# Kernel tuning notes

Measured on AMD Instinct MI355X. Metric: run time of the kernel, lower is better.

The kernel has to match this reference:

```python
import jax, jax.numpy as jnp
import numpy as np

N, E, HS, HBS, L, SH, RBF, T, NZ, NH = 1024, 16384, 128, 32, 5, 25, 32, 50, 10, 4
HD = HS // NH
OUT = 14  # 3x0e + 2x1e + 1x2e -> 3 + 6 + 5
_rng = np.random.default_rng(7)
# fixed Clebsch-Gordan-style coupling tensor and expansion coefficients (deterministic constants)
CG = jnp.asarray((0.1 * _rng.normal(size=(SH, SH, SH))).astype(np.float32))
EXP = jnp.asarray((0.1 * _rng.normal(size=(SH, OUT, OUT))).astype(np.float32))
_SL = [(l * l, 2 * l + 1) for l in range(5)]  # per-l (offset, size) blocks in the 25-dim rep


def _real_sh(d):
    # real spherical harmonics l=0..4 of unit vectors d [E,3] -> [E,25]
    x, y, z = d[:, 0], d[:, 1], d[:, 2]
    x2, y2, z2 = x * x, y * y, z * z
    sh = [0.282095 * jnp.ones_like(x),
          0.488603 * y, 0.488603 * z, 0.488603 * x,
          1.092548 * x * y, 1.092548 * y * z, 0.315392 * (3 * z2 - 1), 1.092548 * x * z, 0.546274 * (x2 - y2),
          0.590044 * y * (3 * x2 - y2), 2.890611 * x * y * z, 0.457046 * y * (5 * z2 - 1),
          0.373176 * z * (5 * z2 - 3), 0.457046 * x * (5 * z2 - 1), 1.445306 * z * (x2 - y2),
          0.590044 * x * (x2 - 3 * y2),
          2.503343 * x * y * (x2 - y2), 1.770131 * y * z * (3 * x2 - y2), 0.946175 * x * y * (7 * z2 - 1),
          0.669047 * y * z * (7 * z2 - 3), 0.105786 * (35 * z2 * z2 - 30 * z2 + 3),
          0.669047 * x * z * (7 * z2 - 3), 0.473087 * (x2 - y2) * (7 * z2 - 1),
          1.770131 * x * z * (x2 - 3 * y2), 0.625836 * (x2 * x2 - 6 * x2 * y2 + y2 * y2)]
    return jnp.stack(sh, axis=-1)


def _rbf(r, cutoff=12.0, alpha=0.5):
    # exponential Bernstein radial basis with cosine cutoff, [E] -> [E,RBF]
    logf = np.concatenate([[0.0], np.cumsum(np.log(np.arange(1, RBF)))])
    logbinom = jnp.asarray((logf[RBF - 1] - logf - logf[::-1]).astype(np.float32))
    k = jnp.arange(RBF, dtype=jnp.float32)
    xr = jnp.exp(-alpha * r)[:, None]
    log1mx = jnp.log1p(-xr + 1e-7)
    b = jnp.exp(logbinom[None] + k[None] * (-alpha * r[:, None]) + (RBF - 1 - k)[None] * log1mx)
    fcut = 0.5 * (jnp.cos(jnp.pi * jnp.clip(r / cutoff, 0.0, 1.0)) + 1.0)
    return b * fcut[:, None]


def _mix(feat, W):
    # per-degree channel mixing: feat [*,C,25], W [5,C,D] -> [*,D,25]
    return jnp.concatenate([jnp.einsum('ncm,cd->ndm', feat[..., o:o + s], W[l])
                            for l, (o, s) in enumerate(_SL)], axis=-1)


def _forward(z, pos, edge_index, batch, t, step, embed, temb_T, temb_H, sig_W1, sig_b1, sig_W2, sig_b2,
             rad_W1, rad_b1, rad_W2, rad_b2, rad_W3, rad_b3, mix_W, Wq, Wk, Wii, Wij, path_ii, path_ij):
    n = z.shape[0]
    e = edge_index.shape[1]
    src, dst = edge_index[0], edge_index[1]
    vec = pos[src] - pos[dst]
    r = jnp.sqrt((vec * vec).sum(-1) + 1e-12)
    dvec = vec / r[:, None]
    rbf = _rbf(r)           # [E,32]
    sh = _real_sh(dvec)     # [E,25]
    nsc = embed[z]          # [N,HS]
    cat = jnp.concatenate([nsc, jnp.tile(temb_T[t][None], (n, 1)), jnp.tile(temb_H[step][None], (n, 1))], axis=-1)
    nsc = jax.nn.relu(cat @ sig_W1 + sig_b1) @ sig_W2 + sig_b2  # sigma_embedding
    x = jnp.zeros((n, HS, SH), jnp.float32).at[:, :, 0].set(nsc)  # scalar-initialized irrep features
    for l in range(L):
        # radial MLP -> per-edge per-channel tensor-product path weights
        h = jax.nn.silu(rbf @ rad_W1[l] + rad_b1[l])
        h = jax.nn.silu(h @ rad_W2[l] + rad_b2[l])
        w = h @ rad_W3[l] + rad_b3[l]                    # [E,HS]
        Tk = jnp.einsum('ej,ijk->eik', sh, CG)           # [E,25,25] CG-coupled SH operator
        msg = jnp.einsum('eci,eik->eck', x[src], Tk) * w[:, :, None]  # per-edge TP message [E,HS,25]
        agg = jax.ops.segment_sum(msg, dst, num_segments=n)
        y = _mix(agg, mix_W[l])
        # equivariant edge attention (scalars drive logits, full irreps are values)
        q = (x[:, :, 0] @ Wq[l]).reshape(n, NH, HD)
        kk = (x[:, :, 0] @ Wk[l]).reshape(n, NH, HD)
        logits = (q[dst] * kk[src]).sum(-1) * (1.0 / float(np.sqrt(HD)))  # [E,NH]
        m = jax.ops.segment_max(logits, dst, num_segments=n)
        m = jnp.where(jnp.isfinite(m), m, 0.0)
        a = jnp.exp(logits - m[dst])
        den = jax.ops.segment_sum(a, dst, num_segments=n)
        alpha = a / (den[dst] + 1e-9)
        v = x[src].reshape(e, NH, HD, SH)
        att = jax.ops.segment_sum(alpha[:, :, None, None] * v, dst, num_segments=n).reshape(n, HS, SH)
        x = x + y + att
        # gate nonlinearity: ssp/silu on scalars, sigmoid gate on higher-l blocks
        g = jax.nn.sigmoid(x[:, :, 0:1])
        x = jnp.concatenate([jax.nn.silu(x[:, :, 0:1]), x[:, :, 1:] * g], axis=-1)
    # expansion to hamiltonian blocks (3x0e+2x1e+1x2e -> 14x14)
    fii = _mix(x, Wii)                    # [N,HBS,25]
    fij = _mix(x[src] + x[dst], Wij)      # [E,HBS,25]
    w_ii = nsc @ path_ii                  # [N,HBS] path weights
    w_ij = jnp.concatenate([nsc[src], nsc[dst]], axis=-1) @ path_ij  # [E,HBS]
    H_ii = jnp.einsum('nd,ndm,mpq->npq', w_ii, fii, EXP)  # [N,14,14]
    H_ij = jnp.einsum('ed,edm,mpq->epq', w_ij, fij, EXP)  # [E,14,14]
    return H_ii, H_ij


def setup_inputs() -> dict:
    key = jax.random.key(0)
    ks = jax.random.split(key, 40)
    def nrm(i, shape, s):
        return (jax.random.normal(ks[i], shape) * s).astype(jnp.float32)
    inp = {}
    inp['z'] = jax.random.randint(ks[0], (N,), 0, NZ)
    inp['pos'] = nrm(1, (N, 3), 3.0)
    inp['edge_index'] = jax.random.randint(ks[2], (2, E), 0, N)
    inp['batch'] = jnp.sort(jax.random.randint(ks[3], (N,), 0, 8))
    inp['t'] = 25
    inp['step'] = 10
    inp['embed'] = nrm(4, (NZ, HS), 1.0)
    inp['temb_T'] = nrm(5, (T, HS), 1.0)
    inp['temb_H'] = nrm(6, (T, HS), 1.0)
    inp['sig_W1'] = nrm(7, (3 * HS, HS), (3 * HS) ** -0.5)
    inp['sig_b1'] = jnp.zeros((HS,), jnp.float32)
    inp['sig_W2'] = nrm(8, (HS, HS), HS ** -0.5)
    inp['sig_b2'] = jnp.zeros((HS,), jnp.float32)
    inp['rad_W1'] = nrm(9, (L, RBF, 64), RBF ** -0.5)
    inp['rad_b1'] = jnp.zeros((L, 64), jnp.float32)
    inp['rad_W2'] = nrm(10, (L, 64, 64), 64 ** -0.5)
    inp['rad_b2'] = jnp.zeros((L, 64), jnp.float32)
    inp['rad_W3'] = nrm(11, (L, 64, HS), 64 ** -0.5)
    inp['rad_b3'] = jnp.zeros((L, HS), jnp.float32)
    inp['mix_W'] = nrm(12, (L, 5, HS, HS), HS ** -0.5)
    inp['Wq'] = nrm(13, (L, HS, HS), HS ** -0.5)
    inp['Wk'] = nrm(14, (L, HS, HS), HS ** -0.5)
    inp['Wii'] = nrm(15, (5, HS, HBS), HS ** -0.5)
    inp['Wij'] = nrm(16, (5, HS, HBS), HS ** -0.5)
    inp['path_ii'] = nrm(17, (HS, HBS), HS ** -0.5)
    inp['path_ij'] = nrm(18, (2 * HS, HBS), (2 * HS) ** -0.5)
    return inp


def reference(z, pos, edge_index, batch, t, step, embed, temb_T, temb_H, sig_W1, sig_b1, sig_W2, sig_b2,
              rad_W1, rad_b1, rad_W2, rad_b2, rad_W3, rad_b3, mix_W, Wq, Wk, Wii, Wij, path_ii, path_ij):
    return _forward(z, pos, edge_index, batch, t, step, embed, temb_T, temb_H, sig_W1, sig_b1, sig_W2, sig_b2,
                    rad_W1, rad_b1, rad_W2, rad_b2, rad_W3, rad_b3, mix_W, Wq, Wk, Wii, Wij, path_ii, path_ij)
```

## Files before the change

kernel.cpp:

```cpp
#include <hip/hip_runtime.h>
#include <cstdint>
#include <cmath>
#include <cstddef>

constexpr int NN   = 1024;
constexpr int NE   = 16384;
constexpr int HSZ  = 128;
constexpr int NSH  = 25;
constexpr int NRBF = 32;
constexpr int NLAY = 5;
constexpr int XSZ  = HSZ * NSH;
constexpr int HII_SZ = NN * 196;


constexpr size_t OFF_CONSTS = 0;
constexpr size_t OFF_X    = 20560;
constexpr size_t OFF_AGG  = OFF_X    + (size_t)NN * XSZ;
constexpr size_t OFF_ATT  = OFF_AGG  + (size_t)NN * XSZ;
constexpr size_t OFF_X0   = OFF_ATT  + (size_t)NN * XSZ;
constexpr size_t OFF_NSC  = OFF_X0   + (size_t)NN * HSZ;
constexpr size_t OFF_Q    = OFF_NSC  + (size_t)NN * HSZ;
constexpr size_t OFF_K    = OFF_Q    + (size_t)NN * HSZ;
constexpr size_t OFF_RBF  = OFF_K    + (size_t)NN * HSZ;
constexpr size_t OFF_SH   = OFF_RBF  + (size_t)NE * NRBF;
constexpr size_t OFF_TK   = OFF_SH   + (size_t)NE * NSH;
constexpr size_t OFF_WRAD = OFF_TK   + (size_t)NE * NSH * NSH;
constexpr size_t OFF_INT  = OFF_WRAD + (size_t)NE * HSZ;
constexpr size_t NEED_BYTES = OFF_INT * 4 + (size_t)(1024 + 1025 + 1024 + 16384) * 4;

namespace qhc {

struct Pcg64 {
  unsigned __int128 state, inc;
  static unsigned __int128 mult() {
    return (((unsigned __int128)2549297995355413924ULL) << 64) | 4865540595714422341ULL;
  }
  void step() { state = state * mult() + inc; }
  uint64_t next64() {
    step();
    uint64_t hi = (uint64_t)(state >> 64), lo = (uint64_t)state;
    uint64_t x = hi ^ lo;
    unsigned rot = (unsigned)(state >> 122);
    return (x >> rot) | (x << ((64u - rot) & 63u));
  }
  double nextd() { return (double)(next64() >> 11) * (1.0 / 9007199254740992.0); }
};

struct HostConsts {
  float buf[20560];
  HostConsts() {
    const uint32_t INIT_A = 0x43b0d7e5u, MULT_A = 0x931e8875u;
    const uint32_t INIT_B = 0x8b51f9ddu, MULT_B = 0x58f38dedu;
    uint32_t pool[4];
    uint32_t hc = INIT_A;
    auto hashf = [&](uint32_t v) -> uint32_t {
      v ^= hc; hc *= MULT_A; v *= hc; v ^= v >> 16; return v;
    };
    auto mixf = [](uint32_t x, uint32_t y) -> uint32_t {
      uint32_t r = x * 0xca01f9ddu - y * 0x4973f715u;
      r ^= r >> 16;
      return r;
    };
    pool[0] = hashf(7u);
    for (int i = 1; i < 4; i++) pool[i] = hashf(0u);
    for (int s = 0; s < 4; s++)
      for (int d = 0; d < 4; d++)
        if (s != d) pool[d] = mixf(pool[d], hashf(pool[s]));
    uint32_t st32[8];
    uint32_t hb = INIT_B;
    for (int i = 0; i < 8; i++) {
      uint32_t v = pool[i % 4];
      v ^= hb; hb *= MULT_B; v *= hb; v ^= v >> 16;
      st32[i] = v;
    }
    uint64_t w0 = st32[0] | ((uint64_t)st32[1] << 32);
    uint64_t w1 = st32[2] | ((uint64_t)st32[3] << 32);
    uint64_t w2 = st32[4] | ((uint64_t)st32[5] << 32);
    uint64_t w3 = st32[6] | ((uint64_t)st32[7] << 32);
    unsigned __int128 seed = (((unsigned __int128)w0) << 64) | w1;
    unsigned __int128 incs = (((unsigned __int128)w2) << 64) | w3;
    Pcg64 g;
    g.state = 0; g.inc = (incs << 1) | 1;
    g.step(); g.state += seed; g.step();
    double wi[256], fi[256]; uint64_t ki[256];
    {
      const double m1 = 4503599627370496.0;
      double dn = 3.6541528853610087963519472518, tn = dn, vn = 0.00492867323399941;
      double q = vn / std::exp(-0.5 * dn * dn);
      ki[0] = (uint64_t)((dn / q) * m1); ki[1] = 0;
      wi[0] = q / m1; wi[255] = dn / m1;
      fi[0] = 1.0; fi[255] = std::exp(-0.5 * dn * dn);
      for (int i = 254; i >= 1; i--) {
        dn = std::sqrt(-2.0 * std::log(vn / dn + std::exp(-0.5 * dn * dn)));
        ki[i + 1] = (uint64_t)((dn / tn) * m1);
        tn = dn;
        fi[i] = std::exp(-0.5 * dn * dn);
        wi[i] = dn / m1;
      }
    }
    const double ZR = 3.6541528853610087963519472518;
    const double ZIR = 0.27366123732975827203338247596;
    auto stdnorm = [&]() -> double {
      for (;;) {
        uint64_t r = g.next64();
        int idx = (int)(r & 0xff);
        r >>= 8;
        int sign = (int)(r & 1);
        uint64_t rabs = (r >> 1) & 0x000fffffffffffffULL;
        double xv = (double)rabs * wi[idx];
        if (sign) xv = -xv;
        if (rabs < ki[idx]) return xv;
        if (idx == 0) {
          for (;;) {
            double xx = -ZIR * std::log1p(-g.nextd());
            double yy = -std::log1p(-g.nextd());
            if (yy + yy > xx * xx)
              return ((rabs >> 8) & 1) ? -(ZR + xx) : (ZR + xx);
          }
        } else {
          if (((fi[idx - 1] - fi[idx]) * g.nextd() + fi[idx]) < std::exp(-0.5 * xv * xv))
            return xv;
        }
      }
    };
    for (int i = 0; i < 15625 + 4900; i++) buf[i] = (float)(0.1 * stdnorm());
    double logf[32]; logf[0] = 0.0;
    for (int i = 1; i < 32; i++) logf[i] = logf[i - 1] + std::log((double)i);
    for (int k = 0; k < 32; k++) buf[15625 + 4900 + k] = (float)(logf[31] - logf[k] - logf[31 - k]);
    buf[20557] = buf[20558] = buf[20559] = 0.f;
  }
};
static HostConsts g_hc;
}

__device__ __forceinline__ float siluf(float a) { return a / (1.f + expf(-a)); }

__global__ __launch_bounds__(256) void qh_geom(
    const float* __restrict__ pos, const int* __restrict__ ei,
    const float* __restrict__ lbn, float* __restrict__ rbf, float* __restrict__ sh) {
  int e = blockIdx.x * 256 + threadIdx.x;
  if (e >= NE) return;
  int s = ei[e], d = ei[NE + e];
  float vx = pos[s * 3 + 0] - pos[d * 3 + 0];
  float vy = pos[s * 3 + 1] - pos[d * 3 + 1];
  float vz = pos[s * 3 + 2] - pos[d * 3 + 2];
  float r = sqrtf(vx * vx + vy * vy + vz * vz + 1e-12f);
  float inv = 1.0f / r;
  float x = vx * inv, y = vy * inv, z = vz * inv;
  float x2 = x * x, y2 = y * y, z2 = z * z;
  float* sp = sh + (size_t)e * NSH;
  sp[0] = 0.282095f;
  sp[1] = 0.488603f * y;
  sp[2] = 0.488603f * z;
  sp[3] = 0.488603f * x;
  sp[4] = 1.092548f * x * y;
  sp[5] = 1.092548f * y * z;
  sp[6] = 0.315392f * (3.f * z2 - 1.f);
  sp[7] = 1.092548f * x * z;
  sp[8] = 0.546274f * (x2 - y2);
  sp[9] = 0.590044f * y * (3.f * x2 - y2);
  sp[10] = 2.890611f * x * y * z;
  sp[11] = 0.457046f * y * (5.f * z2 - 1.f);
  sp[12] = 0.373176f * z * (5.f * z2 - 3.f);
  sp[13] = 0.457046f * x * (5.f * z2 - 1.f);
  sp[14] = 1.445306f * z * (x2 - y2);
  sp[15] = 0.590044f * x * (x2 - 3.f * y2);
  sp[16] = 2.503343f * x * y * (x2 - y2);
  sp[17] = 1.770131f * y * z * (3.f * x2 - y2);
  sp[18] = 0.946175f * x * y * (7.f * z2 - 1.f);
  sp[19] = 0.669047f * y * z * (7.f * z2 - 3.f);
  sp[20] = 0.105786f * (35.f * z2 * z2 - 30.f * z2 + 3.f);
  sp[21] = 0.669047f * x * z * (7.f * z2 - 3.f);
  sp[22] = 0.473087f * (x2 - y2) * (7.f * z2 - 1.f);
  sp[23] = 1.770131f * x * z * (x2 - 3.f * y2);
  sp[24] = 0.625836f * (x2 * x2 - 6.f * x2 * y2 + y2 * y2);
  float xr = expf(-0.5f * r);
  float l1 = log1pf(-xr + 1e-7f);
  float fc = 0.5f * (cosf(3.14159265358979323846f * fminf(r * (1.0f / 12.0f), 1.0f)) + 1.0f);
  float* rp = rbf + (size_t)e * NRBF;
  for (int k = 0; k < NRBF; k++) {
    float b = expf(lbn[k] + (float)k * (-0.5f * r) + (float)(NRBF - 1 - k) * l1);
    rp[k] = b * fc;
  }
}

__global__ __launch_bounds__(256) void qh_tk(
    const float* __restrict__ sh, const float* __restrict__ CG, float* __restrict__ Tk) {
  __shared__ float shl[32 * NSH];
  int e0 = blockIdx.x * 32;
  int t = threadIdx.x;
  for (int i = t; i < 32 * NSH; i += 256) shl[i] = sh[(size_t)e0 * NSH + i];
  __syncthreads();
  for (int ik = t; ik < NSH * NSH; ik += 256) {
    int i = ik / NSH, k = ik % NSH;
    float cg[NSH];
#pragma unroll
    for (int j = 0; j < NSH; j++) cg[j] = CG[i * 625 + j * NSH + k];
    for (int ee = 0; ee < 32; ee++) {
      float acc = 0.f;
#pragma unroll
      for (int j = 0; j < NSH; j++) acc += shl[ee * NSH + j] * cg[j];
      Tk[(size_t)(e0 + ee) * 625 + ik] = acc;
    }
  }
}

__global__ __launch_bounds__(128) void qh_nsc(
    const int* __restrict__ z, const int* __restrict__ tptr, const int* __restrict__ sptr,
    const float* __restrict__ embed, const float* __restrict__ tT, const float* __restrict__ tH,
    const float* __restrict__ W1, const float* __restrict__ b1,
    const float* __restrict__ W2, const float* __restrict__ b2,
    float* __restrict__ nsc, float* __restrict__ x, float* __restrict__ x0) {
  __shared__ float cat[384];
  __shared__ float h[128];
  int nd = blockIdx.x, d = threadIdx.x;
  int zz = z[nd], tt = tptr[0], st = sptr[0];
  cat[d] = embed[zz * HSZ + d];
  cat[128 + d] = tT[tt * HSZ + d];
  cat[256 + d] = tH[st * HSZ + d];
  __syncthreads();
  float a = b1[d];
  for (int c = 0; c < 384; c++) a += cat[c] * W1[c * HSZ + d];
  h[d] = fmaxf(a, 0.f);
  __syncthreads();
  a = b2[d];
  for (int c = 0; c < 128; c++) a += h[c] * W2[c * HSZ + d];
  nsc[nd * HSZ + d] = a;
  x0[nd * HSZ + d] = a;
  float* xr = x + (size_t)nd * XSZ + d;
  xr[0] = a;
  for (int m = 1; m < NSH; m++) xr[m * 128] = 0.f;
}

__global__ __launch_bounds__(256) void qh_zero(int* counts) {
  int i = blockIdx.x * 256 + threadIdx.x;
  if (i < NN) counts[i] = 0;
}
__global__ __launch_bounds__(256) void qh_count(const int* __restrict__ ei, int* counts) {
  int e = blockIdx.x * 256 + threadIdx.x;
  if (e < NE) atomicAdd(&counts[ei[NE + e]], 1);
}
__global__ __launch_bounds__(1024) void qh_scan(const int* __restrict__ counts,
                                                int* starts, int* cursor) {
  __shared__ int tmp[NN];
  int t = threadIdx.x;
  tmp[t] = counts[t];
  __syncthreads();
  for (int ofs = 1; ofs < NN; ofs <<= 1) {
    int v = (t >= ofs) ? tmp[t - ofs] : 0;
    __syncthreads();
    tmp[t] += v;
    __syncthreads();
  }
  starts[t + 1] = tmp[t];
  if (t == 0) starts[0] = 0;
  cursor[t] = (t == 0) ? 0 : tmp[t - 1];
}
__global__ __launch_bounds__(256) void qh_scatter(const int* __restrict__ ei,
                                                  int* cursor, int* perm) {
  int e = blockIdx.x * 256 + threadIdx.x;
  if (e < NE) {
    int d = ei[NE + e];
    int pos = atomicAdd(&cursor[d], 1);
    perm[pos] = e;
  }
}

__global__ __launch_bounds__(256) void qh_rad(
    const float* __restrict__ rbf,
    const float* __restrict__ W1, const float* __restrict__ b1,
    const float* __restrict__ W2, const float* __restrict__ b2,
    const float* __restrict__ W3, const float* __restrict__ b3,
    float* __restrict__ wrad) {
  __shared__ float w1l[2048], w2l[4096], w3l[8192];
  __shared__ float rl[4][32], h1[4][64], h2[4][64];
  int t = threadIdx.x;
  for (int i = t; i < 2048; i += 256) w1l[i] = W1[i];
  for (int i = t; i < 4096; i += 256) w2l[i] = W2[i];
  for (int i = t; i < 8192; i += 256) w3l[i] = W3[i];
  __syncthreads();
  int e0 = blockIdx.x * 16;
  for (int q = 0; q < 4; q++) {
    int eb = e0 + q * 4;
    if (t < 128) rl[t >> 5][t & 31] = rbf[(size_t)(eb + (t >> 5)) * NRBF + (t & 31)];
    __syncthreads();
    {
      int eg = t >> 6, u = t & 63;
      float a = b1[u];
      for (int c = 0; c < 32; c++) a += rl[eg][c] * w1l[c * 64 + u];
      h1[eg][u] = siluf(a);
    }
    __syncthreads();
    {
      int eg = t >> 6, u = t & 63;
      float a = b2[u];
      for (int c = 0; c < 64; c++) a += h1[eg][c] * w2l[c * 64 + u];
      h2[eg][u] = siluf(a);
    }
    __syncthreads();
#pragma unroll
    for (int p = 0; p < 2; p++) {
      int eg = (t >> 7) + p * 2, u = t & 127;
      float a = b3[u];
      for (int c = 0; c < 64; c++) a += h2[eg][c] * w3l[c * 128 + u];
      wrad[(size_t)(eb + eg) * HSZ + u] = a;
    }
    __syncthreads();
  }
}

__global__ __launch_bounds__(256) void qh_qk(
    const float* __restrict__ x0, const float* __restrict__ Wq, const float* __restrict__ Wk,
    float* __restrict__ q, float* __restrict__ kk) {
  __shared__ float xl[128];
  int nd = blockIdx.x, t = threadIdx.x;
  if (t < 128) xl[t] = x0[nd * HSZ + t];
  __syncthreads();
  int d = t & 127;
  const float* W = (t < 128) ? Wq : Wk;
  float a = 0.f;
  for (int c = 0; c < 128; c++) a += xl[c] * W[c * HSZ + d];
  if (t < 128) q[nd * HSZ + d] = a;
  else kk[nd * HSZ + d] = a;
}

__global__ __launch_bounds__(256) void qh_logit(
    const float* __restrict__ q, const float* __restrict__ kk,
    const int* __restrict__ ei, float* __restrict__ logits) {
  int t = threadIdx.x;
  int e = blockIdx.x * 2 + (t >> 7);
  int c = t & 127;
  int s = ei[e], d = ei[NE + e];
  float p = q[d * HSZ + c] * kk[s * HSZ + c];
#pragma unroll
  for (int m = 16; m >= 1; m >>= 1) p += __shfl_xor(p, m);
  if ((c & 31) == 0) logits[e * 4 + (c >> 5)] = p * 0.17677669529663687f;
}

__global__ __launch_bounds__(64) void qh_soft(
    const float* __restrict__ logits, const int* __restrict__ starts,
    const int* __restrict__ perm, float* __restrict__ alpha) {
  int nd = blockIdx.x, t = threadIdx.x;
  int hh = t >> 4, l = t & 15;
  int jb = starts[nd], je = starts[nd + 1];
  float m = -1e30f;
  for (int j = jb + l; j < je; j += 16) m = fmaxf(m, logits[perm[j] * 4 + hh]);
#pragma unroll
  for (int s = 1; s < 16; s <<= 1) m = fmaxf(m, __shfl_xor(m, s));
  float den = 0.f;
  for (int j = jb + l; j < je; j += 16) den += expf(logits[perm[j] * 4 + hh] - m);
#pragma unroll
  for (int s = 1; s < 16; s <<= 1) den += __shfl_xor(den, s);
  float inv = 1.f / (den + 1e-9f);
  for (int j = jb + l; j < je; j += 16) {
    int e = perm[j];
    alpha[e * 4 + hh] = expf(logits[e * 4 + hh] - m) * inv;
  }
}

__global__ __launch_bounds__(256) void qh_msgatt(
    const float* __restrict__ x, const float* __restrict__ Tk,
    const float* __restrict__ wrad, const float* __restrict__ alpha,
    const int* __restrict__ starts, const int* __restrict__ perm,
    const int* __restrict__ ei,
    float* __restrict__ agg, float* __restrict__ att) {
  __shared__ float xs[2][1600];
  __shared__ float tkl[2][628];
  __shared__ float wl[2][64];
  int nd = blockIdx.x >> 1, h = blockIdx.x & 1;
  int t = threadIdx.x;
  int cl = t & 63, q4 = t >> 6;
  int c = h * 64 + cl;
  int k0 = (q4 == 0) ? 0 : (1 + 6 * q4);
  int nk = (q4 == 0) ? 7 : 6;
  float am[7], aa[7];
#pragma unroll
  for (int u = 0; u < 7; u++) { am[u] = 0.f; aa[u] = 0.f; }
  int jb = starts[nd], je = starts[nd + 1];
  float rx[7], rt[3], rw = 0.f;
  if (jb < je) {
    int e = perm[jb], s = ei[e];
#pragma unroll
    for (int u = 0; u < 6; u++) {
      int i = t + u * 256;
      rx[u] = x[(size_t)s * XSZ + (i >> 6) * 128 + h * 64 + (i & 63)];
    }
    if (t < 64) rx[6] = x[(size_t)s * XSZ + 24 * 128 + h * 64 + t];
    rt[0] = Tk[(size_t)e * 625 + t];
    rt[1] = Tk[(size_t)e * 625 + 256 + t];
    if (t < 113) rt[2] = Tk[(size_t)e * 625 + 512 + t];
    if (t < 64) rw = wrad[(size_t)e * HSZ + h * 64 + t];
#pragma unroll
    for (int u = 0; u < 6; u++) xs[0][t + u * 256] = rx[u];
    if (t < 64) xs[0][1536 + t] = rx[6];
    tkl[0][t] = rt[0];
    tkl[0][256 + t] = rt[1];
    if (t < 113) tkl[0][512 + t] = rt[2];
    if (t < 64) wl[0][t] = rw;
  }
  __syncthreads();
  for (int j = jb; j < je; j++) {
    int cur = (j - jb) & 1, nxt = cur ^ 1;
    int e = perm[j];
    float al = alpha[e * 4 + (c >> 5)];
    bool more = (j + 1 < je);
    if (more) {
      int e2 = perm[j + 1], s2 = ei[e2];
#pragma unroll
      for (int u = 0; u < 6; u++) {
        int i = t + u * 256;
        rx[u] = x[(size_t)s2 * XSZ + (i >> 6) * 128 + h * 64 + (i & 63)];
      }
      if (t < 64) rx[6] = x[(size_t)s2 * XSZ + 24 * 128 + h * 64 + t];
      rt[0] = Tk[(size_t)e2 * 625 + t];
      rt[1] = Tk[(size_t)e2 * 625 + 256 + t];
      if (t < 113) rt[2] = Tk[(size_t)e2 * 625 + 512 + t];
      if (t < 64) rw = wrad[(size_t)e2 * HSZ + h * 64 + t];
    }
    float wc = wl[cur][cl];
#pragma unroll
    for (int i = 0; i < NSH; i++) {
      float xw = xs[cur][i * 64 + cl] * wc;
      const float* tr = &tkl[cur][i * 25 + k0];
#pragma unroll
      for (int u = 0; u < 7; u++)
        if (u < nk) am[u] += xw * tr[u];
    }
#pragma unroll
    for (int u = 0; u < 7; u++)
      if (u < nk) aa[u] += al * xs[cur][(k0 + u) * 64 + cl];
    __syncthreads();
    if (more) {
#pragma unroll
      for (int u = 0; u < 6; u++) xs[nxt][t + u * 256] = rx[u];
      if (t < 64) xs[nxt][1536 + t] = rx[6];
      tkl[nxt][t] = rt[0];
      tkl[nxt][256 + t] = rt[1];
      if (t < 113) tkl[nxt][512 + t] = rt[2];
      if (t < 64) wl[nxt][t] = rw;
    }
    __syncthreads();
  }
#pragma unroll
  for (int u = 0; u < 7; u++)
    if (u < nk) {
      agg[(size_t)nd * XSZ + (k0 + u) * 128 + c] = am[u];
      att[(size_t)nd * XSZ + (k0 + u) * 128 + c] = aa[u];
    }
}

__global__ __launch_bounds__(256) void qh_mixgemm(
    const float* __restrict__ mixW, float* __restrict__ agg) {
  __shared__ float Wl[8192];
  __shared__ float Al[4096];
  int b = blockIdx.x, t = threadIdx.x;
  int lb, cum;
  if (b < 32)       { lb = 0; cum = 0; }
  else if (b < 128) { lb = 1; cum = 32; }
  else if (b < 288) { lb = 2; cum = 128; }
  else if (b < 512) { lb = 3; cum = 288; }
  else              { lb = 4; cum = 512; }
  int sl = 2 * lb + 1, o = lb * lb;
  int row0 = (b - cum) * 32;
  const float* W = mixW + lb * 16384;
  for (int i = t; i < 4096; i += 256) {
    int r = i >> 7, cc = i & 127;
    int gr = row0 + r, n = gr / sl, m = o + gr - n * sl;
    Al[i] = agg[(size_t)n * XSZ + m * 128 + cc];
  }
  int dl = t & 63, rg = t >> 6;
  float out[2][8];
  for (int p = 0; p < 2; p++) {
    __syncthreads();
    for (int i = t; i < 8192; i += 256) {
      int cc = i >> 6, d2 = i & 63;
      Wl[i] = W[cc * 128 + p * 64 + d2];
    }
    __syncthreads();
    float acc[8];
#pragma unroll
    for (int r = 0; r < 8; r++) acc[r] = 0.f;
    for (int cc = 0; cc < 128; cc++) {
      float w = Wl[cc * 64 + dl];
#pragma unroll
      for (int r = 0; r < 8; r++) acc[r] += Al[(rg * 8 + r) * 128 + cc] * w;
    }
#pragma unroll
    for (int r = 0; r < 8; r++) out[p][r] = acc[r];
  }
#pragma unroll
  for (int p = 0; p < 2; p++)
#pragma unroll
    for (int r = 0; r < 8; r++) {
      int gr = row0 + rg * 8 + r, n = gr / sl, m = o + gr - n * sl;
      agg[(size_t)n * XSZ + m * 128 + p * 64 + dl] = out[p][r];
    }
}

__global__ __launch_bounds__(256) void qh_gate(
    const float* __restrict__ y, const float* __restrict__ att,
    float* __restrict__ x, float* __restrict__ x0) {
  __shared__ float v0l[128];
  int nd = blockIdx.x, t = threadIdx.x;
  int d = t & 127, mh = t >> 7;
  int m0 = mh ? 13 : 0, nm = mh ? 12 : 13;
  float v[13];
  size_t base = (size_t)nd * XSZ + (size_t)m0 * 128 + d;
#pragma unroll
  for (int u = 0; u < 13; u++)
    if (u < nm) v[u] = x[base + (size_t)u * 128] + y[base + (size_t)u * 128] + att[base + (size_t)u * 128];
  if (mh == 0) v0l[d] = v[0];
  __syncthreads();
  float g = 1.f / (1.f + expf(-v0l[d]));
#pragma unroll
  for (int u = 0; u < 13; u++)
    if (u < nm) x[base + (size_t)u * 128] = v[u] * g;
  if (mh == 0) x0[nd * HSZ + d] = v[0] * g;
}

__global__ __launch_bounds__(256) void qh_prep(
    const float* __restrict__ x, const float* __restrict__ nsc,
    const float* __restrict__ Wii, const float* __restrict__ Wij,
    const float* __restrict__ pii, const float* __restrict__ pij,
    const float* __restrict__ EXPc,
    float* __restrict__ fm, float* __restrict__ awb, float* __restrict__ out) {
  __shared__ float xl[XSZ];
  __shared__ float nl[128];
  __shared__ float wc[4096];
  __shared__ float fml[800];
  __shared__ float wiil[32];
  __shared__ float gl[25];
  int nd = blockIdx.x, t = threadIdx.x;
  for (int i = t; i < XSZ; i += 256) xl[i] = x[(size_t)nd * XSZ + i];
  if (t < 128) nl[t] = nsc[nd * HSZ + t];
  __syncthreads();
  if (t < 32) {
    float a = 0.f;
    for (int cc = 0; cc < 128; cc++) a += nl[cc] * pii[cc * 32 + t];
    wiil[t] = a;
  } else if (t < 96) {
    int d = (t - 32) & 31;
    int half = (t - 32) >> 5;
    const float* pp = pij + (half ? 128 * 32 : 0);
    float a = 0.f;
    for (int cc = 0; cc < 128; cc++) a += nl[cc] * pp[cc * 32 + d];
    awb[nd * 64 + half * 32 + d] = a;
  }
  for (int lb = 0; lb < 5; lb++) {
    __syncthreads();
    for (int i = t; i < 4096; i += 256) wc[i] = Wii[lb * 4096 + i];
    __syncthreads();
    int o = lb * lb, sl = 2 * lb + 1;
    for (int idx = t; idx < 32 * sl; idx += 256) {
      int d = idx & 31, m = o + (idx >> 5);
      float a = 0.f;
      for (int cc = 0; cc < 128; cc++) a += xl[m * 128 + cc] * wc[cc * 32 + d];
      fml[d * NSH + m] = a;
    }
  }
  __syncthreads();
  if (t < 25) {
    float a = 0.f;
#pragma unroll
    for (int d = 0; d < 32; d++) a += wiil[d] * fml[d * NSH + t];
    gl[t] = a;
  }
  __syncthreads();
  if (t < 196) {
    float a = 0.f;
#pragma unroll
    for (int m = 0; m < 25; m++) a += gl[m] * EXPc[m * 196 + t];
    out[(size_t)nd * 196 + t] = a;
  }
  for (int lb = 0; lb < 5; lb++) {
    __syncthreads();
    for (int i = t; i < 4096; i += 256) wc[i] = Wij[lb * 4096 + i];
    __syncthreads();
    int o = lb * lb, sl = 2 * lb + 1;
    for (int idx = t; idx < 32 * sl; idx += 256) {
      int d = idx & 31, m = o + (idx >> 5);
      float a = 0.f;
      for (int cc = 0; cc < 128; cc++) a += xl[m * 128 + cc] * wc[cc * 32 + d];
      fm[(size_t)nd * 800 + d * NSH + m] = a;
    }
  }
}

__global__ __launch_bounds__(256) void qh_fij2(
    const int* __restrict__ ei, const float* __restrict__ fm,
    const float* __restrict__ awb, const float* __restrict__ EXPc,
    float* __restrict__ out) {
  __shared__ float fsum[800], wsum[32], gl[25];
  int e = blockIdx.x, t = threadIdx.x;
  int s = ei[e], d2 = ei[NE + e];
  for (int i = t; i < 800; i += 256)
    fsum[i] = fm[(size_t)s * 800 + i] + fm[(size_t)d2 * 800 + i];
  if (t < 32) wsum[t] = awb[s * 64 + t] + awb[d2 * 64 + 32 + t];
  __syncthreads();
  if (t < 25) {
    float a = 0.f;
#pragma unroll
    for (int d = 0; d < 32; d++) a += wsum[d] * fsum[d * NSH + t];
    gl[t] = a;
  }
  __syncthreads();
  if (t < 196) {
    float a = 0.f;
#pragma unroll
    for (int m = 0; m < 25; m++) a += gl[m] * EXPc[m * 196 + t];
    out[HII_SZ + (size_t)e * 196 + t] = a;
  }
}

extern "C" void kernel_launch(void* const* d_in, const int* in_sizes, int n_in,
                              void* d_out, int out_size, void* d_ws, size_t ws_size,
                              hipStream_t stream) {
  (void)in_sizes; (void)n_in; (void)out_size;
  if (ws_size < NEED_BYTES) return;

  const int*   z    = (const int*)d_in[0];
  const float* pos  = (const float*)d_in[1];
  const int*   ei   = (const int*)d_in[2];
  const int*   tptr = (const int*)d_in[4];
  const int*   sptr = (const int*)d_in[5];
  const float* embed= (const float*)d_in[6];
  const float* tT   = (const float*)d_in[7];
  const float* tH   = (const float*)d_in[8];
  const float* sW1  = (const float*)d_in[9];
  const float* sb1  = (const float*)d_in[10];
  const float* sW2  = (const float*)d_in[11];
  const float* sb2  = (const float*)d_in[12];
  const float* rW1  = (const float*)d_in[13];
  const float* rb1  = (const float*)d_in[14];
  const float* rW2  = (const float*)d_in[15];
  const float* rb2  = (const float*)d_in[16];
  const float* rW3  = (const float*)d_in[17];
  const float* rb3  = (const float*)d_in[18];
  const float* mixW = (const float*)d_in[19];
  const float* Wq   = (const float*)d_in[20];
  const float* Wk   = (const float*)d_in[21];
  const float* Wii  = (const float*)d_in[22];
  const float* Wij  = (const float*)d_in[23];
  const float* pii  = (const float*)d_in[24];
  const float* pij  = (const float*)d_in[25];

  float* ws = (float*)d_ws;
  float* CGd   = ws + OFF_CONSTS;
  float* EXPd  = CGd + 15625;
  float* LBNd  = CGd + 15625 + 4900;
  float* x     = ws + OFF_X;
  float* agg   = ws + OFF_AGG;
  float* att   = ws + OFF_ATT;
  float* x0    = ws + OFF_X0;
  float* nsc   = ws + OFF_NSC;
  float* qarr  = ws + OFF_Q;
  float* karr  = ws + OFF_K;
  float* rbf   = ws + OFF_RBF;
  float* sh    = ws + OFF_SH;
  float* Tk    = ws + OFF_TK;
  float* wrad  = ws + OFF_WRAD;
  float* logits = ws + OFF_SH;
  float* alphaA = ws + OFF_SH + 65536;
  float* fm     = ws + OFF_AGG;
  float* awb    = ws + OFF_AGG + 819200;
  int* ibase   = (int*)(ws + OFF_INT);
  int* counts  = ibase;
  int* starts  = ibase + 1024;
  int* cursor  = ibase + 1024 + 1025;
  int* perm    = ibase + 1024 + 1025 + 1024;
  float* outp  = (float*)d_out;

  hipMemcpyAsync(CGd, qhc::g_hc.buf, 20557 * sizeof(float), hipMemcpyHostToDevice, stream);

  qh_geom<<<NE / 256, 256, 0, stream>>>(pos, ei, LBNd, rbf, sh);
  qh_tk<<<NE / 32, 256, 0, stream>>>(sh, CGd, Tk);
  qh_nsc<<<NN, 128, 0, stream>>>(z, tptr, sptr, embed, tT, tH, sW1, sb1, sW2, sb2, nsc, x, x0);
  qh_zero<<<NN / 256, 256, 0, stream>>>(counts);
  qh_count<<<NE / 256, 256, 0, stream>>>(ei, counts);
  qh_scan<<<1, 1024, 0, stream>>>(counts, starts, cursor);
  qh_scatter<<<NE / 256, 256, 0, stream>>>(ei, cursor, perm);

  for (int l = 0; l < NLAY; l++) {
    qh_rad<<<NE / 16, 256, 0, stream>>>(rbf,
        rW1 + (size_t)l * 32 * 64, rb1 + (size_t)l * 64,
        rW2 + (size_t)l * 64 * 64, rb2 + (size_t)l * 64,
        rW3 + (size_t)l * 64 * 128, rb3 + (size_t)l * 128, wrad);
    qh_qk<<<NN, 256, 0, stream>>>(x0, Wq + (size_t)l * 16384, Wk + (size_t)l * 16384, qarr, karr);
    qh_logit<<<NE / 2, 256, 0, stream>>>(qarr, karr, ei, logits);
    qh_soft<<<NN, 64, 0, stream>>>(logits, starts, perm, alphaA);
    qh_msgatt<<<NN * 2, 256, 0, stream>>>(x, Tk, wrad, alphaA, starts, perm, ei, agg, att);
    qh_mixgemm<<<800, 256, 0, stream>>>(mixW + (size_t)l * 81920, agg);
    qh_gate<<<NN, 256, 0, stream>>>(agg, att, x, x0);
  }

  qh_prep<<<NN, 256, 0, stream>>>(x, nsc, Wii, Wij, pii, pij, EXPd, fm, awb, outp);
  qh_fij2<<<NE, 256, 0, stream>>>(ei, fm, awb, EXPd, outp);
}
```

Measured before the change: 1.486 ms.

## Restructure message-attention kernel to one block per node with float4 channels; simplify radial MLP

The message/attention kernel now uses one block per destination node instead of two half-channel blocks. Each thread holds 4 channels as float4 and 3-4 output components, and attention weights are prefetched into shared memory alongside the edge data. This halves the redundant Tk and edge-metadata loads per node and widens memory accesses, at the cost of fewer blocks (1024) and more registers per thread. The radial MLP kernel drops its 56KB shared-memory weight staging, processes 4 edges per block, and reads weights straight from global/L2. That trades reuse for occupancy and less staging overhead.

```diff
diff --git a/kernel.cpp b/kernel.cpp
--- a/kernel.cpp
+++ b/kernel.cpp
@@ -272,40 +272,31 @@
     const float* __restrict__ W2, const float* __restrict__ b2,
     const float* __restrict__ W3, const float* __restrict__ b3,
     float* __restrict__ wrad) {
-  __shared__ float w1l[2048], w2l[4096], w3l[8192];
-  __shared__ float rl[4][32], h1[4][64], h2[4][64];
+  __shared__ float rl[4][32];
+  __shared__ float h1[4][64];
+  __shared__ float h2[4][64];
   int t = threadIdx.x;
-  for (int i = t; i < 2048; i += 256) w1l[i] = W1[i];
-  for (int i = t; i < 4096; i += 256) w2l[i] = W2[i];
-  for (int i = t; i < 8192; i += 256) w3l[i] = W3[i];
-  __syncthreads();
-  int e0 = blockIdx.x * 16;
-  for (int q = 0; q < 4; q++) {
-    int eb = e0 + q * 4;
-    if (t < 128) rl[t >> 5][t & 31] = rbf[(size_t)(eb + (t >> 5)) * NRBF + (t & 31)];
-    __syncthreads();
-    {
-      int eg = t >> 6, u = t & 63;
-      float a = b1[u];
-      for (int c = 0; c < 32; c++) a += rl[eg][c] * w1l[c * 64 + u];
-      h1[eg][u] = siluf(a);
-    }
-    __syncthreads();
-    {
-      int eg = t >> 6, u = t & 63;
-      float a = b2[u];
-      for (int c = 0; c < 64; c++) a += h1[eg][c] * w2l[c * 64 + u];
-      h2[eg][u] = siluf(a);
-    }
-    __syncthreads();
-#pragma unroll
-    for (int p = 0; p < 2; p++) {
-      int eg = (t >> 7) + p * 2, u = t & 127;
-      float a = b3[u];
-      for (int c = 0; c < 64; c++) a += h2[eg][c] * w3l[c * 128 + u];
-      wrad[(size_t)(eb + eg) * HSZ + u] = a;
-    }
-    __syncthreads();
+  int eg = t >> 6, u = t & 63;
+  int e = blockIdx.x * 4 + eg;
+  if (t < 128) rl[t >> 5][t & 31] = rbf[(size_t)(blockIdx.x * 4 + (t >> 5)) * NRBF + (t & 31)];
+  __syncthreads();
+  float a = b1[u];
+#pragma unroll 8
+  for (int c = 0; c < 32; c++) a += rl[eg][c] * W1[c * 64 + u];
+  h1[eg][u] = siluf(a);
+  __syncthreads();
+  a = b2[u];
+#pragma unroll 8
+  for (int c = 0; c < 64; c++) a += h1[eg][c] * W2[c * 64 + u];
+  h2[eg][u] = siluf(a);
+  __syncthreads();
+#pragma unroll
+  for (int p = 0; p < 2; p++) {
+    int uu = u + p * 64;
+    float o = b3[uu];
+#pragma unroll 8
+    for (int c = 0; c < 64; c++) o += h2[eg][c] * W3[c * 128 + uu];
+    wrad[(size_t)e * HSZ + uu] = o;
   }
 }
 
@@ -364,88 +355,95 @@
     const int* __restrict__ starts, const int* __restrict__ perm,
     const int* __restrict__ ei,
     float* __restrict__ agg, float* __restrict__ att) {
-  __shared__ float xs[2][1600];
+  __shared__ float4 xs4[2][800];
   __shared__ float tkl[2][628];
-  __shared__ float wl[2][64];
-  int nd = blockIdx.x >> 1, h = blockIdx.x & 1;
-  int t = threadIdx.x;
-  int cl = t & 63, q4 = t >> 6;
-  int c = h * 64 + cl;
-  int k0 = (q4 == 0) ? 0 : (1 + 6 * q4);
-  int nk = (q4 == 0) ? 7 : 6;
-  float am[7], aa[7];
-#pragma unroll
-  for (int u = 0; u < 7; u++) { am[u] = 0.f; aa[u] = 0.f; }
+  __shared__ float wl[2][128];
+  __shared__ float alf[2][4];
+  int nd = blockIdx.x, t = threadIdx.x;
+  int cg = t & 31, kg = t >> 5;
+  int c0 = cg * 4;
+  int k0 = (kg == 0) ? 0 : (3 * kg + 1);
+  int nk = (kg == 0) ? 4 : 3;
+  float4 am[4], aa[4];
+#pragma unroll
+  for (int u = 0; u < 4; u++) {
+    am[u] = make_float4(0.f, 0.f, 0.f, 0.f);
+    aa[u] = make_float4(0.f, 0.f, 0.f, 0.f);
+  }
   int jb = starts[nd], je = starts[nd + 1];
-  float rx[7], rt[3], rw = 0.f;
+  float4 rx[4];
+  float rt[3], rw = 0.f, ral = 0.f;
   if (jb < je) {
     int e = perm[jb], s = ei[e];
-#pragma unroll
-    for (int u = 0; u < 6; u++) {
-      int i = t + u * 256;
-      rx[u] = x[(size_t)s * XSZ + (i >> 6) * 128 + h * 64 + (i & 63)];
-    }
-    if (t < 64) rx[6] = x[(size_t)s * XSZ + 24 * 128 + h * 64 + t];
-    rt[0] = Tk[(size_t)e * 625 + t];
-    rt[1] = Tk[(size_t)e * 625 + 256 + t];
-    if (t < 113) rt[2] = Tk[(size_t)e * 625 + 512 + t];
-    if (t < 64) rw = wrad[(size_t)e * HSZ + h * 64 + t];
-#pragma unroll
-    for (int u = 0; u < 6; u++) xs[0][t + u * 256] = rx[u];
-    if (t < 64) xs[0][1536 + t] = rx[6];
-    tkl[0][t] = rt[0];
-    tkl[0][256 + t] = rt[1];
+    const float4* xsrc = (const float4*)(x + (size_t)s * XSZ);
+    rx[0] = xsrc[t]; rx[1] = xsrc[t + 256]; rx[2] = xsrc[t + 512];
+    if (t < 32) rx[3] = xsrc[t + 768];
+    const float* tks = Tk + (size_t)e * 625;
+    rt[0] = tks[t]; rt[1] = tks[256 + t];
+    if (t < 113) rt[2] = tks[512 + t];
+    if (t < 128) rw = wrad[(size_t)e * HSZ + t];
+    if (t < 4) ral = alpha[e * 4 + t];
+    xs4[0][t] = rx[0]; xs4[0][t + 256] = rx[1]; xs4[0][t + 512] = rx[2];
+    if (t < 32) xs4[0][t + 768] = rx[3];
+    tkl[0][t] = rt[0]; tkl[0][256 + t] = rt[1];
     if (t < 113) tkl[0][512 + t] = rt[2];
-    if (t < 64) wl[0][t] = rw;
+    if (t < 128) wl[0][t] = rw;
+    if (t < 4) alf[0][t] = ral;
   }
   __syncthreads();
   for (int j = jb; j < je; j++) {
     int cur = (j - jb) & 1, nxt = cur ^ 1;
-    int e = perm[j];
-    float al = alpha[e * 4 + (c >> 5)];
     bool more = (j + 1 < je);
     if (more) {
       int e2 = perm[j + 1], s2 = ei[e2];
-#pragma unroll
-      for (int u = 0; u < 6; u++) {
-        int i = t + u * 256;
-        rx[u] = x[(size_t)s2 * XSZ + (i >> 6) * 128 + h * 64 + (i & 63)];
+      const float4* xsrc = (const float4*)(x + (size_t)s2 * XSZ);
+      rx[0] = xsrc[t]; rx[1] = xsrc[t + 256]; rx[2] = xsrc[t + 512];
+      if (t < 32) rx[3] = xsrc[t + 768];
+      const float* tks = Tk + (size_t)e2 * 625;
+      rt[0] = tks[t]; rt[1] = tks[256 + t];
+      if (t < 113) rt[2] = tks[512 + t];
+      if (t < 128) rw = wrad[(size_t)e2 * HSZ + t];
+      if (t < 4) ral = alpha[e2 * 4 + t];
+    }
+    float4 wc4 = *(const float4*)&wl[cur][c0];
+    float al = alf[cur][cg >> 3];
+    const float* tb = &tkl[cur][k0];
+#pragma unroll
+    for (int i = 0; i < NSH; i++) {
+      float4 x4 = xs4[cur][i * 32 + cg];
+      float4 xw;
+      xw.x = x4.x * wc4.x; xw.y = x4.y * wc4.y;
+      xw.z = x4.z * wc4.z; xw.w = x4.w * wc4.w;
+      const float* tr = tb + i * 25;
+#pragma unroll
+      for (int u = 0; u < 4; u++) {
+        float tv = tr[u];
+        am[u].x += xw.x * tv; am[u].y += xw.y * tv;
+        am[u].z += xw.z * tv; am[u].w += xw.w * tv;
       }
-      if (t < 64) rx[6] = x[(size_t)s2 * XSZ + 24 * 128 + h * 64 + t];
-      rt[0] = Tk[(size_t)e2 * 625 + t];
-      rt[1] = Tk[(size_t)e2 * 625 + 256 + t];
-      if (t < 113) rt[2] = Tk[(size_t)e2 * 625 + 512 + t];
-      if (t < 64) rw = wrad[(size_t)e2 * HSZ + h * 64 + t];
-    }
-    float wc = wl[cur][cl];
-#pragma unroll
-    for (int i = 0; i < NSH; i++) {
-      float xw = xs[cur][i * 64 + cl] * wc;
-      const float* tr = &tkl[cur][i * 25 + k0];
-#pragma unroll
-      for (int u = 0; u < 7; u++)
-        if (u < nk) am[u] += xw * tr[u];
-    }
-#pragma unroll
-    for (int u = 0; u < 7; u++)
-      if (u < nk) aa[u] += al * xs[cur][(k0 + u) * 64 + cl];
+      int di = i - k0;
+      if (di >= 0 && di < nk) {
+        aa[di].x += al * x4.x; aa[di].y += al * x4.y;
+        aa[di].z += al * x4.z; aa[di].w += al * x4.w;
+      }
+    }
     __syncthreads();
     if (more) {
-#pragma unroll
-      for (int u = 0; u < 6; u++) xs[nxt][t + u * 256] = rx[u];
-      if (t < 64) xs[nxt][1536 + t] = rx[6];
-      tkl[nxt][t] = rt[0];
-      tkl[nxt][256 + t] = rt[1];
+      xs4[nxt][t] = rx[0]; xs4[nxt][t + 256] = rx[1]; xs4[nxt][t + 512] = rx[2];
+      if (t < 32) xs4[nxt][t + 768] = rx[3];
+      tkl[nxt][t] = rt[0]; tkl[nxt][256 + t] = rt[1];
       if (t < 113) tkl[nxt][512 + t] = rt[2];
-      if (t < 64) wl[nxt][t] = rw;
-    }
-    __syncthreads();
-  }
-#pragma unroll
-  for (int u = 0; u < 7; u++)
+      if (t < 128) wl[nxt][t] = rw;
+      if (t < 4) alf[nxt][t] = ral;
+    }
+    __syncthreads();
+  }
+  size_t base = (size_t)nd * XSZ + c0;
+#pragma unroll
+  for (int u = 0; u < 4; u++)
     if (u < nk) {
-      agg[(size_t)nd * XSZ + (k0 + u) * 128 + c] = am[u];
-      att[(size_t)nd * XSZ + (k0 + u) * 128 + c] = aa[u];
+      *(float4*)(agg + base + (size_t)(k0 + u) * 128) = am[u];
+      *(float4*)(att + base + (size_t)(k0 + u) * 128) = aa[u];
     }
 }
 
@@ -681,14 +679,14 @@
   qh_scatter<<<NE / 256, 256, 0, stream>>>(ei, cursor, perm);
 
   for (int l = 0; l < NLAY; l++) {
-    qh_rad<<<NE / 16, 256, 0, stream>>>(rbf,
+    qh_rad<<<NE / 4, 256, 0, stream>>>(rbf,
         rW1 + (size_t)l * 32 * 64, rb1 + (size_t)l * 64,
         rW2 + (size_t)l * 64 * 64, rb2 + (size_t)l * 64,
         rW3 + (size_t)l * 64 * 128, rb3 + (size_t)l * 128, wrad);
     qh_qk<<<NN, 256, 0, stream>>>(x0, Wq + (size_t)l * 16384, Wk + (size_t)l * 16384, qarr, karr);
     qh_logit<<<NE / 2, 256, 0, stream>>>(qarr, karr, ei, logits);
     qh_soft<<<NN, 64, 0, stream>>>(logits, starts, perm, alphaA);
-    qh_msgatt<<<NN * 2, 256, 0, stream>>>(x, Tk, wrad, alphaA, starts, perm, ei, agg, att);
+    qh_msgatt<<<NN, 256, 0, stream>>>(x, Tk, wrad, alphaA, starts, perm, ei, agg, att);
     qh_mixgemm<<<800, 256, 0, stream>>>(mixW + (size_t)l * 81920, agg);
     qh_gate<<<NN, 256, 0, stream>>>(agg, att, x, x0);
   }
```

Measured after the change: 2.501 ms. 68.4% more time.
